# Optimization experiments

Hardware: AMD Instinct MI355X
Metric: run time of the kernel (lower is better)

Reference implementation:

```python
import jax, jax.numpy as jnp
import numpy as np

N_NODES = 100000
N_EDGES = 1000000
IN, HID, HEADS, OUT = 256, 32, 4, 40
HH = HID * HEADS  # 128
NEG_SLOPE = 0.2


def gat_conv(x, W, al, ar, b, src, dst, heads):
    """DGL-style GATConv. x:[N,Din] W:[Din,heads*F] al/ar/b:[heads,F]. Returns [N,heads,F]."""
    N = x.shape[0]
    h = (x @ W).reshape(N, heads, -1)                      # [N,H,F]
    el = (h * al).sum(-1)                                  # [N,H]
    er = (h * ar).sum(-1)                                  # [N,H]
    e = jax.nn.leaky_relu(el[src] + er[dst], NEG_SLOPE)    # [E,H]
    # segment softmax over incoming edges of each dst node
    m = jax.ops.segment_max(e, dst, num_segments=N)        # [N,H]
    m = jnp.where(jnp.isfinite(m), m, 0.0)                 # nodes w/o in-edges
    ex = jnp.exp(e - m[dst])                               # [E,H]
    s = jax.ops.segment_sum(ex, dst, num_segments=N)       # [N,H]
    alpha = ex / jnp.where(s[dst] == 0, 1.0, s[dst])       # [E,H]
    out = jax.ops.segment_sum(alpha[:, :, None] * h[src], dst, num_segments=N)
    return out + b                                          # [N,H,F]


def setup_inputs() -> dict:
    key = jax.random.key(0)
    ks = jax.random.split(key, 12)
    p = lambda k, shape, fan: jax.random.normal(k, shape, jnp.float32) / np.float32(np.sqrt(fan))
    features = jax.random.normal(ks[0], (N_NODES, IN), jnp.float32)
    src = jax.random.randint(ks[1], (N_EDGES,), 0, N_NODES, jnp.int32)
    dst = jax.random.randint(ks[2], (N_EDGES,), 0, N_NODES, jnp.int32)
    W1 = p(ks[3], (IN, HH), IN)
    al1 = p(ks[4], (HEADS, HID), HID)
    ar1 = p(ks[5], (HEADS, HID), HID)
    b1 = jnp.zeros((HEADS, HID), jnp.float32)
    W2 = p(ks[6], (HH, HH), HH)
    al2 = p(ks[7], (HEADS, HID), HID)
    ar2 = p(ks[8], (HEADS, HID), HID)
    b2 = jnp.zeros((HEADS, HID), jnp.float32)
    W3 = p(ks[9], (HH, OUT), HH)
    al3 = p(ks[10], (1, OUT), OUT)
    ar3 = p(ks[11], (1, OUT), OUT)
    b3 = jnp.zeros((1, OUT), jnp.float32)
    return dict(features=features, W1=W1, al1=al1, ar1=ar1, b1=b1,
                W2=W2, al2=al2, ar2=ar2, b2=b2,
                W3=W3, al3=al3, ar3=ar3, b3=b3, src=src, dst=dst)


def reference(features, W1, al1, ar1, b1, W2, al2, ar2, b2, W3, al3, ar3, b3, src, dst):
    N = features.shape[0]
    h = jax.nn.relu(gat_conv(features, W1, al1, ar1, b1, src, dst, HEADS).reshape(N, -1))
    h = jax.nn.relu(gat_conv(h, W2, al2, ar2, b2, src, dst, HEADS).reshape(N, -1))
    # dropout: eval mode -> identity
    h = gat_conv(h, W3, al3, ar3, b3, src, dst, 1).mean(1)  # [N,OUT]
    return jax.nn.log_softmax(h, axis=1)
```

## Files before the change

kernel.cpp:

```cpp
#include <hip/hip_runtime.h>
#include <hip/hip_bf16.h>
#include <math.h>

#define NN 100000
#define NE 1000000
#define NPB 512
#define NBUC ((NN + NPB - 1) / NPB)
#define CAPB 8192
#define P1B 512
#define P1E ((NE + P1B - 1) / P1B)
#define BCAP 512

typedef __attribute__((ext_vector_type(8))) short bf16x8;
typedef __attribute__((ext_vector_type(4))) float f32x4;
typedef unsigned int u32;
typedef unsigned short u16;
typedef unsigned long long u64;

__device__ __forceinline__ u16 f2b(float f) {
    __hip_bfloat16 h = __float2bfloat16(f);
    return *reinterpret_cast<u16*>(&h);
}
__device__ __forceinline__ float b2f(u16 u) {
    __hip_bfloat16 h = *reinterpret_cast<__hip_bfloat16*>(&u);
    return __bfloat162float(h);
}
__device__ __forceinline__ float bflo(u32 v) { return __uint_as_float(v << 16); }
__device__ __forceinline__ float bfhi(u32 v) { return __uint_as_float(v & 0xffff0000u); }


__global__ void bucket_cnt(const int* __restrict__ dst, int* __restrict__ bcnt, int E) {
    __shared__ int c[NBUC];
    for (int i = threadIdx.x; i < NBUC; i += 256) c[i] = 0;
    __syncthreads();
    int i = blockIdx.x * 256 + threadIdx.x;
    const int stride = gridDim.x * 256;
    for (; i < E; i += stride) atomicAdd(&c[dst[i] >> 9], 1);
    __syncthreads();
    for (int j = threadIdx.x; j < NBUC; j += 256)
        if (c[j]) atomicAdd(&bcnt[j], c[j]);
}

__global__ void bucket_scan(const int* __restrict__ bcnt, int* __restrict__ bbase,
                            int* __restrict__ gcur) {
    __shared__ int s[256];
    const int tid = threadIdx.x;
    int v = (tid < NBUC) ? bcnt[tid] : 0;
    s[tid] = v;
    __syncthreads();
    for (int off = 1; off < 256; off <<= 1) {
        int t = (tid >= off) ? s[tid - off] : 0;
        __syncthreads();
        s[tid] += t;
        __syncthreads();
    }
    if (tid < NBUC) {
        int excl = s[tid] - v;
        bbase[tid] = excl;
        gcur[tid] = excl;
    }
    if (tid == NBUC - 1) bbase[NBUC] = s[tid];
}


__global__ __launch_bounds__(256) void part1(const int* __restrict__ src,
                                             const int* __restrict__ dst,
                                             int* __restrict__ gcur,
                                             long long* __restrict__ ebuf) {
    __shared__ int cnt[256], sex[256], base[256], cur2[256], scn[256];
    __shared__ long long stage[P1E];
    const int tid = threadIdx.x;
    const int e0 = blockIdx.x * P1E;
    const int e1 = min(e0 + P1E, NE);
    cnt[tid] = 0;
    __syncthreads();
    for (int i = e0 + tid; i < e1; i += 256)
        atomicAdd(&cnt[dst[i] >> 9], 1);
    __syncthreads();
    int v = cnt[tid];
    scn[tid] = v;
    __syncthreads();
    #pragma unroll
    for (int off = 1; off < 256; off <<= 1) {
        int t = (tid >= off) ? scn[tid - off] : 0;
        __syncthreads();
        scn[tid] += t;
        __syncthreads();
    }
    sex[tid] = scn[tid] - v;
    if (tid < NBUC) base[tid] = (v > 0) ? atomicAdd(&gcur[tid], v) : 0;
    cur2[tid] = 0;
    __syncthreads();
    for (int i = e0 + tid; i < e1; i += 256) {
        int d = dst[i], s = src[i];
        int b = d >> 9;
        int slot = sex[b] + atomicAdd(&cur2[b], 1);
        stage[slot] = ((long long)(u32)d << 32) | (u32)s;
    }
    __syncthreads();
    const int tot = e1 - e0;
    for (int i = tid; i < tot; i += 256) {
        long long ll = stage[i];
        int b = (int)((u64)ll >> 32) >> 9;
        ebuf[(size_t)base[b] + (i - sex[b])] = ll;
    }
}

__global__ __launch_bounds__(256) void part2B(const int* __restrict__ bbase,
                                              const long long* __restrict__ ebuf,
                                              int* __restrict__ rowptr,
                                              int* __restrict__ csrc) {
    __shared__ int nb[NPB], cnt[NPB];
    __shared__ int stage[CAPB];
    __shared__ int ssum[256];
    const int tid = threadIdx.x;
    const int n0 = blockIdx.x << 9;
    const int nn = min(NPB, NN - n0);
    const int estart = bbase[blockIdx.x];
    const int eend = bbase[blockIdx.x + 1];
    const int tot = eend - estart;
    for (int i = tid; i < NPB; i += 256) cnt[i] = 0;
    __syncthreads();
    for (int i = estart + tid; i < eend; i += 256) {
        int ln = (int)((u64)ebuf[i] >> 32) - n0;
        atomicAdd(&cnt[ln], 1);
    }
    __syncthreads();
    int a = cnt[2 * tid], b = cnt[2 * tid + 1];
    int ts = a + b;
    ssum[tid] = ts;
    __syncthreads();
    #pragma unroll
    for (int off = 1; off < 256; off <<= 1) {
        int t = (tid >= off) ? ssum[tid - off] : 0;
        __syncthreads();
        ssum[tid] += t;
        __syncthreads();
    }
    int eb = ssum[tid] - ts;
    nb[2 * tid] = eb;
    nb[2 * tid + 1] = eb + a;
    if (2 * tid < nn)     rowptr[n0 + 2 * tid]     = estart + eb;
    if (2 * tid + 1 < nn) rowptr[n0 + 2 * tid + 1] = estart + eb + a;
    if (tid == 0 && blockIdx.x == gridDim.x - 1) rowptr[NN] = eend;
    __syncthreads();
    for (int i = tid; i < NPB; i += 256) cnt[i] = 0;
    __syncthreads();
    if (tot <= CAPB) {
        for (int i = estart + tid; i < eend; i += 256) {
            long long ll = ebuf[i];
            int ln = (int)((u64)ll >> 32) - n0;
            int pos = nb[ln] + atomicAdd(&cnt[ln], 1);
            stage[pos] = (int)ll;
        }
        __syncthreads();
        for (int i = tid; i < tot; i += 256) csrc[estart + i] = stage[i];
    } else {
        for (int i = estart + tid; i < eend; i += 256) {
            long long ll = ebuf[i];
            int ln = (int)((u64)ll >> 32) - n0;
            int pos = nb[ln] + atomicAdd(&cnt[ln], 1);
            csrc[estart + pos] = (int)ll;
        }
    }
}


__global__ void transW3(const float* __restrict__ W1, u16* __restrict__ W1t,
                        const float* __restrict__ W2, u16* __restrict__ W2t,
                        const float* __restrict__ W3, u16* __restrict__ W3t) {
    int idx = blockIdx.x * 256 + threadIdx.x;
    if (idx < 32768) {
        int n = idx / 256, k = idx % 256;
        W1t[idx] = f2b(W1[(size_t)k * 128 + n]);
    } else if (idx < 32768 + 16384) {
        int j = idx - 32768;
        int n = j / 128, k = j % 128;
        W2t[j] = f2b(W2[(size_t)k * 128 + n]);
    } else if (idx < 32768 + 16384 + 6144) {
        int j = idx - 32768 - 16384;
        int n = j / 128, k = j % 128;
        W3t[j] = f2b((n < 40) ? W3[(size_t)k * 40 + n] : 0.f);
    }
}

template<int K, int NT, int OUTW, bool AF32, int NH>
__global__ __launch_bounds__(256, 4) void gemm_s(const void* __restrict__ Ap_,
                                                 const u16* __restrict__ Wt,
                                                 const float* __restrict__ al,
                                                 const float* __restrict__ ar,
                                                 u16* __restrict__ C,
                                                 float* __restrict__ el,
                                                 float* __restrict__ er, int M) {
    constexpr int KC = 128;
    constexpr int NKC = K / KC;
    constexpr int NB = NT * 16;
    constexpr int CHK = KC / 8;
    __shared__ u16 lB[NB * KC];
    const int tid = threadIdx.x;
    const int w = tid >> 6, l = tid & 63;
    const int lr = l & 15, lq = l >> 4;
    const int row0 = blockIdx.x * 64 + w * 16;
    const u16* Ab = (const u16*)Ap_;
    const float* Af = (const float*)Ap_;

    int gr0 = row0 + lr; if (gr0 >= M) gr0 = M - 1;
    const size_t aoff = (size_t)gr0 * K;

    f32x4 acc[NT] = {};
    #pragma unroll
    for (int kc = 0; kc < NKC; ++kc) {
        for (int idx = tid; idx < NB * CHK; idx += 256) {
            int row = idx / CHK, c = idx % CHK;
            float4 v = *reinterpret_cast<const float4*>(&Wt[(size_t)row * K + kc * KC + c * 8]);
            int cs = c ^ (row & 7);
            *reinterpret_cast<float4*>(&lB[row * KC + cs * 8]) = v;
        }
        __syncthreads();
        bf16x8 a0, a1, a2, a3;
        if (AF32) {
            float4 v[8];
            #pragma unroll
            for (int i = 0; i < 8; ++i)
                v[i] = *reinterpret_cast<const float4*>(
                    &Af[aoff + kc * KC + (i >> 1) * 32 + lq * 8 + (i & 1) * 4]);
            bf16x8 t[4];
            #pragma unroll
            for (int i = 0; i < 4; ++i) {
                t[i][0] = (short)f2b(v[2 * i].x); t[i][1] = (short)f2b(v[2 * i].y);
                t[i][2] = (short)f2b(v[2 * i].z); t[i][3] = (short)f2b(v[2 * i].w);
                t[i][4] = (short)f2b(v[2 * i + 1].x); t[i][5] = (short)f2b(v[2 * i + 1].y);
                t[i][6] = (short)f2b(v[2 * i + 1].z); t[i][7] = (short)f2b(v[2 * i + 1].w);
            }
            a0 = t[0]; a1 = t[1]; a2 = t[2]; a3 = t[3];
        } else {
            a0 = *reinterpret_cast<const bf16x8*>(&Ab[aoff + kc * KC + 0 * 32 + lq * 8]);
            a1 = *reinterpret_cast<const bf16x8*>(&Ab[aoff + kc * KC + 1 * 32 + lq * 8]);
            a2 = *reinterpret_cast<const bf16x8*>(&Ab[aoff + kc * KC + 2 * 32 + lq * 8]);
            a3 = *reinterpret_cast<const bf16x8*>(&Ab[aoff + kc * KC + 3 * 32 + lq * 8]);
        }
        #pragma unroll
        for (int ks = 0; ks < 4; ++ks) {
            bf16x8 aF = (ks == 0) ? a0 : (ks == 1) ? a1 : (ks == 2) ? a2 : a3;
            const int cs = (ks * 4 + lq) ^ (lr & 7);
            #pragma unroll
            for (int nr = 0; nr < NT; ++nr) {
                bf16x8 bF = *reinterpret_cast<const bf16x8*>(&lB[(nr * 16 + lr) * KC + cs * 8]);
                acc[nr] = __builtin_amdgcn_mfma_f32_16x16x32_bf16(aF, bF, acc[nr], 0, 0, 0);
            }
        }
        if (kc + 1 < NKC) __syncthreads();
    }

    float alv[NT], arv[NT];
    #pragma unroll
    for (int nr = 0; nr < NT; ++nr) {
        int c = nr * 16 + lr;
        alv[nr] = (c < OUTW) ? al[c] : 0.f;
        arv[nr] = (c < OUTW) ? ar[c] : 0.f;
    }
    #pragma unroll
    for (int reg = 0; reg < 4; ++reg) {
        int gr = row0 + lq * 4 + reg;
        bool ok = gr < M;
        if (ok) {
            #pragma unroll
            for (int nr = 0; nr < NT; ++nr) {
                int gc = nr * 16 + lr;
                if (gc < OUTW) C[(size_t)gr * OUTW + gc] = f2b(acc[nr][reg]);
            }
        }
        float pl[NH] = {}, pr[NH] = {};
        #pragma unroll
        for (int nr = 0; nr < NT; ++nr) {
            int hidx = (NH == 1) ? 0 : (nr >> 1);
            pl[hidx] = fmaf(acc[nr][reg], alv[nr], pl[hidx]);
            pr[hidx] = fmaf(acc[nr][reg], arv[nr], pr[hidx]);
        }
        #pragma unroll
        for (int o = 8; o >= 1; o >>= 1) {
            #pragma unroll
            for (int hh = 0; hh < NH; ++hh) {
                pl[hh] += __shfl_xor(pl[hh], o);
                pr[hh] += __shfl_xor(pr[hh], o);
            }
        }
        if (ok && lr == 0) {
            #pragma unroll
            for (int hh = 0; hh < NH; ++hh) {
                el[gr * NH + hh] = pl[hh];
                er[gr * NH + hh] = pr[hh];
            }
        }
    }
}


template<bool RELU>
__global__ __launch_bounds__(256) void agg4v6(const char* __restrict__ hbase,
                                              const float4* __restrict__ el4,
                                              const float4* __restrict__ er4,
                                              const float* __restrict__ bias,
                                              const int* __restrict__ rowptr,
                                              const int* __restrict__ csrc,
                                              u32* __restrict__ out, int N) {
    __shared__ u32 s_ed[BCAP][8];
    __shared__ int s_off[9];
    const int tid = threadIdx.x, w = tid >> 6, lane = tid & 63;
    const int base = blockIdx.x * 8;
    if (tid < 9) {
        int n = base + tid;
        s_off[tid] = rowptr[n <= N ? n : N];
    }
    __syncthreads();
    const int beg_blk = s_off[0];
    const int T = s_off[8] - beg_blk;
    const int hh = lane >> 4;
    const u32 lshl = (u32)(lane << 2);
    const float2 bv = reinterpret_cast<const float2*>(bias)[lane];
    const bool small = (T <= BCAP);

    if (small) {
        for (int t = tid; t < T; t += 256) {
            int sid = csrc[beg_blk + t];
            int nd = 0;
            #pragma unroll
            for (int k = 1; k < 8; ++k) nd += (t >= (s_off[k] - beg_blk)) ? 1 : 0;
            float4 er = er4[base + nd];
            float4 ev = el4[sid];
            float e0 = ev.x + er.x; e0 = e0 > 0.f ? e0 : 0.2f * e0;
            float e1 = ev.y + er.y; e1 = e1 > 0.f ? e1 : 0.2f * e1;
            float e2 = ev.z + er.z; e2 = e2 > 0.f ? e2 : 0.2f * e2;
            float e3 = ev.w + er.w; e3 = e3 > 0.f ? e3 : 0.2f * e3;
            u32 so = (u32)sid << 8;
            *reinterpret_cast<int2*>(&s_ed[t][0]) = make_int2(__float_as_int(__expf(e0)), (int)so);
            *reinterpret_cast<int2*>(&s_ed[t][2]) = make_int2(__float_as_int(__expf(e1)), (int)so);
            *reinterpret_cast<int2*>(&s_ed[t][4]) = make_int2(__float_as_int(__expf(e2)), (int)so);
            *reinterpret_cast<int2*>(&s_ed[t][6]) = make_int2(__float_as_int(__expf(e3)), (int)so);
        }
    }
    __syncthreads();

    const int nA = base + 2 * w;
    if (nA >= N) return;
    const int nB = nA + 1;
    float aA[4] = {}, bA[4] = {}, sA[4] = {};
    float aB[4] = {}, bB[4] = {}, sB[4] = {};

    if (small) {
        const int oA0 = s_off[2 * w] - beg_blk, oA1 = s_off[2 * w + 1] - beg_blk;
        const int oB0 = oA1, oB1 = s_off[2 * w + 2] - beg_blk;
        const int dA = oA1 - oA0, dB = oB1 - oB0;
        const int it = max((dA + 3) >> 2, (dB + 3) >> 2);
        for (int i = 0; i < it; ++i) {
            const int pA = oA0 + i * 4, pB = oB0 + i * 4;
            #pragma unroll
            for (int k = 0; k < 4; ++k) {
                int j = pA + k; bool v = j < oA1;
                int2 rv = *reinterpret_cast<const int2*>(&s_ed[v ? j : 0][hh * 2]);
                float wg = v ? __int_as_float(rv.x) : 0.f;
                u32 hv = *reinterpret_cast<const u32*>(hbase + ((u32)rv.y | lshl));
                aA[k] = fmaf(wg, bflo(hv), aA[k]);
                bA[k] = fmaf(wg, bfhi(hv), bA[k]);
                sA[k] += wg;
            }
            #pragma unroll
            for (int k = 0; k < 4; ++k) {
                int j = pB + k; bool v = j < oB1;
                int2 rv = *reinterpret_cast<const int2*>(&s_ed[v ? j : 0][hh * 2]);
                float wg = v ? __int_as_float(rv.x) : 0.f;
                u32 hv = *reinterpret_cast<const u32*>(hbase + ((u32)rv.y | lshl));
                aB[k] = fmaf(wg, bflo(hv), aB[k]);
                bB[k] = fmaf(wg, bfhi(hv), bB[k]);
                sB[k] += wg;
            }
        }
        {
            float accA = (aA[0] + aA[1]) + (aA[2] + aA[3]);
            float accB = (bA[0] + bA[1]) + (bA[2] + bA[3]);
            float s = (sA[0] + sA[1]) + (sA[2] + sA[3]);
            float invs = (dA > 0) ? 1.f / s : 0.f;
            float oA = accA * invs + bv.x;
            float oB = accB * invs + bv.y;
            if (RELU) { oA = fmaxf(oA, 0.f); oB = fmaxf(oB, 0.f); }
            out[(size_t)nA * 64 + lane] = ((u32)f2b(oB) << 16) | (u32)f2b(oA);
        }
        {
            float accA = (aB[0] + aB[1]) + (aB[2] + aB[3]);
            float accB = (bB[0] + bB[1]) + (bB[2] + bB[3]);
            float s = (sB[0] + sB[1]) + (sB[2] + sB[3]);
            float invs = (dB > 0) ? 1.f / s : 0.f;
            float oA = accA * invs + bv.x;
            float oB = accB * invs + bv.y;
            if (RELU) { oA = fmaxf(oA, 0.f); oB = fmaxf(oB, 0.f); }
            if (nB < N)
                out[(size_t)nB * 64 + lane] = ((u32)f2b(oB) << 16) | (u32)f2b(oA);
        }
    } else {
        #pragma unroll
        for (int which = 0; which < 2; ++which) {
            int nd = nA + which;
            if (nd >= N) break;
            int beg = s_off[2 * w + which], end = s_off[2 * w + which + 1];
            float4 er = er4[nd];
            float er_h = hh == 0 ? er.x : hh == 1 ? er.y : hh == 2 ? er.z : er.w;
            float s = 0.f, accA = 0.f, accB = 0.f;
            for (int q = beg; q < end; ++q) {
                int sid = csrc[q];
                float4 ev = el4[sid];
                float e = (hh == 0 ? ev.x : hh == 1 ? ev.y : hh == 2 ? ev.z : ev.w) + er_h;
                e = e > 0.f ? e : 0.2f * e;
                float pe = __expf(e);
                u32 hv = *reinterpret_cast<const u32*>(hbase + (((u32)sid << 8) | lshl));
                s += pe;
                accA = fmaf(pe, bflo(hv), accA);
                accB = fmaf(pe, bfhi(hv), accB);
            }
            float invs = (end > beg) ? 1.f / s : 0.f;
            float oA = accA * invs + bv.x;
            float oB = accB * invs + bv.y;
            if (RELU) { oA = fmaxf(oA, 0.f); oB = fmaxf(oB, 0.f); }
            out[(size_t)nd * 64 + lane] = ((u32)f2b(oB) << 16) | (u32)f2b(oA);
        }
    }
}

__global__ __launch_bounds__(256) void agg1v6(const char* __restrict__ hbase,
                                              const float* __restrict__ el,
                                              const float* __restrict__ er,
                                              const float* __restrict__ bias,
                                              const int* __restrict__ rowptr,
                                              const int* __restrict__ csrc,
                                              float* __restrict__ out, int N) {
    __shared__ u32 s_e1[BCAP][2];
    __shared__ int s_off[9];
    const int tid = threadIdx.x, w = tid >> 6, lane = tid & 63;
    const int base = blockIdx.x * 8;
    if (tid < 9) {
        int n = base + tid;
        s_off[tid] = rowptr[n <= N ? n : N];
    }
    __syncthreads();
    const int beg_blk = s_off[0];
    const int T = s_off[8] - beg_blk;
    const int ll = lane < 40 ? lane : 39;
    const u32 lloff = (u32)(ll << 1);
    const float bvv = (lane < 40) ? bias[lane] : 0.f;
    const bool small = (T <= BCAP);

    if (small) {
        for (int t = tid; t < T; t += 256) {
            int sid = csrc[beg_blk + t];
            int nd = 0;
            #pragma unroll
            for (int k = 1; k < 8; ++k) nd += (t >= (s_off[k] - beg_blk)) ? 1 : 0;
            float e = el[sid] + er[base + nd];
            e = e > 0.f ? e : 0.2f * e;
            *reinterpret_cast<int2*>(&s_e1[t][0]) =
                make_int2(__float_as_int(__expf(e)), (int)((u32)sid * 80u));
        }
    }
    __syncthreads();

    const int nA = base + 2 * w;
    if (nA >= N) return;
    const int nB = nA + 1;
    float aA[4] = {}, sA[4] = {}, aB[4] = {}, sB[4] = {};
    float accA, invsA, accB, invsB;
    bool haveB = (nB < N);

    if (small) {
        const int oA0 = s_off[2 * w] - beg_blk, oA1 = s_off[2 * w + 1] - beg_blk;
        const int oB0 = oA1, oB1 = s_off[2 * w + 2] - beg_blk;
        const int dA = oA1 - oA0, dB = oB1 - oB0;
        const int it = max((dA + 3) >> 2, (dB + 3) >> 2);
        for (int i = 0; i < it; ++i) {
            const int pA = oA0 + i * 4, pB = oB0 + i * 4;
            #pragma unroll
            for (int k = 0; k < 4; ++k) {
                int j = pA + k; bool v = j < oA1;
                int2 rv = *reinterpret_cast<const int2*>(&s_e1[v ? j : 0][0]);
                float wg = v ? __int_as_float(rv.x) : 0.f;
                u16 hv = *reinterpret_cast<const u16*>(hbase + ((u32)rv.y + lloff));
                aA[k] = fmaf(wg, b2f(hv), aA[k]);
                sA[k] += wg;
            }
            #pragma unroll
            for (int k = 0; k < 4; ++k) {
                int j = pB + k; bool v = j < oB1;
                int2 rv = *reinterpret_cast<const int2*>(&s_e1[v ? j : 0][0]);
                float wg = v ? __int_as_float(rv.x) : 0.f;
                u16 hv = *reinterpret_cast<const u16*>(hbase + ((u32)rv.y + lloff));
                aB[k] = fmaf(wg, b2f(hv), aB[k]);
                sB[k] += wg;
            }
        }
        accA = (aA[0] + aA[1]) + (aA[2] + aA[3]);
        float ssA = (sA[0] + sA[1]) + (sA[2] + sA[3]);
        invsA = (dA > 0) ? 1.f / ssA : 0.f;
        accB = (aB[0] + aB[1]) + (aB[2] + aB[3]);
        float ssB = (sB[0] + sB[1]) + (sB[2] + sB[3]);
        invsB = (dB > 0) ? 1.f / ssB : 0.f;
    } else {
        accA = 0.f; accB = 0.f; invsA = 0.f; invsB = 0.f;
        #pragma unroll
        for (int which = 0; which < 2; ++which) {
            int nd = nA + which;
            if (nd >= N) break;
            int beg = s_off[2 * w + which], end = s_off[2 * w + which + 1];
            float ern = er[nd];
            float s = 0.f, acc = 0.f;
            for (int q = beg; q < end; ++q) {
                int sid = csrc[q];
                float e = el[sid] + ern; e = e > 0.f ? e : 0.2f * e;
                float pe = __expf(e);
                u16 hv = *reinterpret_cast<const u16*>(hbase + ((u32)sid * 80u + lloff));
                s += pe;
                acc = fmaf(pe, b2f(hv), acc);
            }
            float inv = (end > beg) ? 1.f / s : 0.f;
            if (which == 0) { accA = acc; invsA = inv; }
            else { accB = acc; invsB = inv; }
        }
    }
    {
        float v = accA * invsA + bvv;
        float vv = (lane < 40) ? v : -INFINITY;
        float mx = vv;
        #pragma unroll
        for (int o = 32; o >= 1; o >>= 1) mx = fmaxf(mx, __shfl_xor(mx, o));
        float ex = (lane < 40) ? __expf(v - mx) : 0.f;
        float se = ex;
        #pragma unroll
        for (int o = 32; o >= 1; o >>= 1) se += __shfl_xor(se, o);
        if (lane < 40) out[(size_t)nA * 40 + lane] = v - mx - logf(se);
    }
    if (haveB) {
        float v = accB * invsB + bvv;
        float vv = (lane < 40) ? v : -INFINITY;
        float mx = vv;
        #pragma unroll
        for (int o = 32; o >= 1; o >>= 1) mx = fmaxf(mx, __shfl_xor(mx, o));
        float ex = (lane < 40) ? __expf(v - mx) : 0.f;
        float se = ex;
        #pragma unroll
        for (int o = 32; o >= 1; o >>= 1) se += __shfl_xor(se, o);
        if (lane < 40) out[(size_t)nB * 40 + lane] = v - mx - logf(se);
    }
}


extern "C" void kernel_launch(void* const* d_in, const int* in_sizes, int n_in,
                              void* d_out, int out_size, void* d_ws, size_t ws_size,
                              hipStream_t stream) {
    const float* feat = (const float*)d_in[0];
    const float* W1  = (const float*)d_in[1];
    const float* al1 = (const float*)d_in[2];
    const float* ar1 = (const float*)d_in[3];
    const float* b1  = (const float*)d_in[4];
    const float* W2  = (const float*)d_in[5];
    const float* al2 = (const float*)d_in[6];
    const float* ar2 = (const float*)d_in[7];
    const float* b2  = (const float*)d_in[8];
    const float* W3  = (const float*)d_in[9];
    const float* al3 = (const float*)d_in[10];
    const float* ar3 = (const float*)d_in[11];
    const float* b3  = (const float*)d_in[12];
    const int*   src = (const int*)d_in[13];
    const int*   dst = (const int*)d_in[14];
    float* out = (float*)d_out;
    const int N = NN, E = NE;

    char* ws = (char*)d_ws;
    size_t off = 0;
    auto alloc = [&](size_t bytes) -> char* {
        char* p = ws + off;
        off += (bytes + 255) & ~(size_t)255;
        return p;
    };
    int* bcnt   = (int*)alloc(256 * 4);
    int* bbase  = (int*)alloc(256 * 4);
    int* gcur   = (int*)alloc(256 * 4);
    int* rowptr = (int*)alloc((size_t)(N + 1) * 4);
    int* csrc   = (int*)alloc((size_t)E * 4);
    long long* ebuf = (long long*)alloc((size_t)E * 8);
    float* el   = (float*)alloc((size_t)N * 4 * 4);
    float* er   = (float*)alloc((size_t)N * 4 * 4);
    u16* hb     = (u16*)alloc((size_t)N * 128 * 2);
    u16* xb     = (u16*)alloc((size_t)N * 128 * 2);
    u16* h3     = (u16*)alloc((size_t)N * 40 * 2 + 256);
    u16* W1t    = (u16*)alloc((size_t)128 * 256 * 2);
    u16* W2t    = (u16*)alloc((size_t)128 * 128 * 2);
    u16* W3t    = (u16*)alloc((size_t)48 * 128 * 2);

    hipMemsetAsync(bcnt, 0, NBUC * 4, stream);
    bucket_cnt<<<1024, 256, 0, stream>>>(dst, bcnt, E);
    bucket_scan<<<1, 256, 0, stream>>>(bcnt, bbase, gcur);
    part1<<<P1B, 256, 0, stream>>>(src, dst, gcur, ebuf);
    part2B<<<NBUC, 256, 0, stream>>>(bbase, ebuf, rowptr, csrc);

    transW3<<<(32768 + 16384 + 6144 + 255) / 256, 256, 0, stream>>>(W1, W1t, W2, W2t, W3, W3t);

    int gemmGrid = (N + 63) / 64;
    int aggGrid = (N + 7) / 8;

    gemm_s<256, 8, 128, true, 4><<<gemmGrid, 256, 0, stream>>>(feat, W1t, al1, ar1, hb, el, er, N);
    agg4v6<true><<<aggGrid, 256, 0, stream>>>((const char*)hb, (const float4*)el, (const float4*)er,
                                              b1, rowptr, csrc, (u32*)xb, N);

    gemm_s<128, 8, 128, false, 4><<<gemmGrid, 256, 0, stream>>>(xb, W2t, al2, ar2, hb, el, er, N);
    agg4v6<true><<<aggGrid, 256, 0, stream>>>((const char*)hb, (const float4*)el, (const float4*)er,
                                              b2, rowptr, csrc, (u32*)xb, N);

    gemm_s<128, 3, 40, false, 1><<<gemmGrid, 256, 0, stream>>>(xb, W3t, al3, ar3, h3, el, er, N);
    agg1v6<<<aggGrid, 256, 0, stream>>>((const char*)h3, el, er, b3, rowptr, csrc, out, N);
}
```

Before: 268.7 us.

## Make GEMM persistent with full weight matrix resident in LDS

```diff
diff --git a/kernel.cpp b/kernel.cpp
--- a/kernel.cpp
+++ b/kernel.cpp
@@ -10,6 +10,7 @@
 #define P1B 512
 #define P1E ((NE + P1B - 1) / P1B)
 #define BCAP 512
+#define GEMM_GB 782
 
 typedef __attribute__((ext_vector_type(8))) short bf16x8;
 typedef __attribute__((ext_vector_type(4))) float f32x4;
@@ -185,7 +186,7 @@
 }
 
 template<int K, int NT, int OUTW, bool AF32, int NH>
-__global__ __launch_bounds__(256, 4) void gemm_s(const void* __restrict__ Ap_,
+__global__ __launch_bounds__(256, 2) void gemm_p(const void* __restrict__ Ap_,
                                                  const u16* __restrict__ Wt,
                                                  const float* __restrict__ al,
                                                  const float* __restrict__ ar,
@@ -195,62 +196,22 @@
     constexpr int KC = 128;
     constexpr int NKC = K / KC;
     constexpr int NB = NT * 16;
-    constexpr int CHK = KC / 8;
-    __shared__ u16 lB[NB * KC];
+    constexpr int CHKF = K / 8;
+    __shared__ u16 lB[NB * K];
     const int tid = threadIdx.x;
     const int w = tid >> 6, l = tid & 63;
     const int lr = l & 15, lq = l >> 4;
-    const int row0 = blockIdx.x * 64 + w * 16;
     const u16* Ab = (const u16*)Ap_;
     const float* Af = (const float*)Ap_;
-
-    int gr0 = row0 + lr; if (gr0 >= M) gr0 = M - 1;
-    const size_t aoff = (size_t)gr0 * K;
-
-    f32x4 acc[NT] = {};
-    #pragma unroll
-    for (int kc = 0; kc < NKC; ++kc) {
-        for (int idx = tid; idx < NB * CHK; idx += 256) {
-            int row = idx / CHK, c = idx % CHK;
-            float4 v = *reinterpret_cast<const float4*>(&Wt[(size_t)row * K + kc * KC + c * 8]);
-            int cs = c ^ (row & 7);
-            *reinterpret_cast<float4*>(&lB[row * KC + cs * 8]) = v;
-        }
-        __syncthreads();
-        bf16x8 a0, a1, a2, a3;
-        if (AF32) {
-            float4 v[8];
-            #pragma unroll
-            for (int i = 0; i < 8; ++i)
-                v[i] = *reinterpret_cast<const float4*>(
-                    &Af[aoff + kc * KC + (i >> 1) * 32 + lq * 8 + (i & 1) * 4]);
-            bf16x8 t[4];
-            #pragma unroll
-            for (int i = 0; i < 4; ++i) {
-                t[i][0] = (short)f2b(v[2 * i].x); t[i][1] = (short)f2b(v[2 * i].y);
-                t[i][2] = (short)f2b(v[2 * i].z); t[i][3] = (short)f2b(v[2 * i].w);
-                t[i][4] = (short)f2b(v[2 * i + 1].x); t[i][5] = (short)f2b(v[2 * i + 1].y);
-                t[i][6] = (short)f2b(v[2 * i + 1].z); t[i][7] = (short)f2b(v[2 * i + 1].w);
-            }
-            a0 = t[0]; a1 = t[1]; a2 = t[2]; a3 = t[3];
-        } else {
-            a0 = *reinterpret_cast<const bf16x8*>(&Ab[aoff + kc * KC + 0 * 32 + lq * 8]);
-            a1 = *reinterpret_cast<const bf16x8*>(&Ab[aoff + kc * KC + 1 * 32 + lq * 8]);
-            a2 = *reinterpret_cast<const bf16x8*>(&Ab[aoff + kc * KC + 2 * 32 + lq * 8]);
-            a3 = *reinterpret_cast<const bf16x8*>(&Ab[aoff + kc * KC + 3 * 32 + lq * 8]);
-        }
-        #pragma unroll
-        for (int ks = 0; ks < 4; ++ks) {
-            bf16x8 aF = (ks == 0) ? a0 : (ks == 1) ? a1 : (ks == 2) ? a2 : a3;
-            const int cs = (ks * 4 + lq) ^ (lr & 7);
-            #pragma unroll
-            for (int nr = 0; nr < NT; ++nr) {
-                bf16x8 bF = *reinterpret_cast<const bf16x8*>(&lB[(nr * 16 + lr) * KC + cs * 8]);
-                acc[nr] = __builtin_amdgcn_mfma_f32_16x16x32_bf16(aF, bF, acc[nr], 0, 0, 0);
-            }
-        }
-        if (kc + 1 < NKC) __syncthreads();
-    }
+    const int numTiles = (M + 63) / 64;
+
+    for (int idx = tid; idx < NB * CHKF; idx += 256) {
+        int row = idx / CHKF, c = idx % CHKF;
+        float4 v = *reinterpret_cast<const float4*>(&Wt[(size_t)row * K + c * 8]);
+        int cs = c ^ (row & 7);
+        *reinterpret_cast<float4*>(&lB[row * K + cs * 8]) = v;
+    }
+    __syncthreads();
 
     float alv[NT], arv[NT];
     #pragma unroll
@@ -259,37 +220,81 @@
         alv[nr] = (c < OUTW) ? al[c] : 0.f;
         arv[nr] = (c < OUTW) ? ar[c] : 0.f;
     }
-    #pragma unroll
-    for (int reg = 0; reg < 4; ++reg) {
-        int gr = row0 + lq * 4 + reg;
-        bool ok = gr < M;
-        if (ok) {
+
+    for (int t = blockIdx.x; t < numTiles; t += GEMM_GB) {
+        const int row0 = t * 64 + w * 16;
+        int gr0 = row0 + lr; if (gr0 >= M) gr0 = M - 1;
+        const size_t aoff = (size_t)gr0 * K;
+
+        f32x4 acc[NT] = {};
+        #pragma unroll
+        for (int kc = 0; kc < NKC; ++kc) {
+            bf16x8 a0, a1, a2, a3;
+            if (AF32) {
+                float4 v[8];
+                #pragma unroll
+                for (int i = 0; i < 8; ++i)
+                    v[i] = *reinterpret_cast<const float4*>(
+                        &Af[aoff + kc * KC + (i >> 1) * 32 + lq * 8 + (i & 1) * 4]);
+                bf16x8 tt[4];
+                #pragma unroll
+                for (int i = 0; i < 4; ++i) {
+                    tt[i][0] = (short)f2b(v[2 * i].x); tt[i][1] = (short)f2b(v[2 * i].y);
+                    tt[i][2] = (short)f2b(v[2 * i].z); tt[i][3] = (short)f2b(v[2 * i].w);
+                    tt[i][4] = (short)f2b(v[2 * i + 1].x); tt[i][5] = (short)f2b(v[2 * i + 1].y);
+                    tt[i][6] = (short)f2b(v[2 * i + 1].z); tt[i][7] = (short)f2b(v[2 * i + 1].w);
+                }
+                a0 = tt[0]; a1 = tt[1]; a2 = tt[2]; a3 = tt[3];
+            } else {
+                a0 = *reinterpret_cast<const bf16x8*>(&Ab[aoff + kc * KC + 0 * 32 + lq * 8]);
+                a1 = *reinterpret_cast<const bf16x8*>(&Ab[aoff + kc * KC + 1 * 32 + lq * 8]);
+                a2 = *reinterpret_cast<const bf16x8*>(&Ab[aoff + kc * KC + 2 * 32 + lq * 8]);
+                a3 = *reinterpret_cast<const bf16x8*>(&Ab[aoff + kc * KC + 3 * 32 + lq * 8]);
+            }
+            #pragma unroll
+            for (int ks = 0; ks < 4; ++ks) {
+                bf16x8 aF = (ks == 0) ? a0 : (ks == 1) ? a1 : (ks == 2) ? a2 : a3;
+                const int cs = ((kc * 16 + ks * 4 + lq) ^ (lr & 7));
+                #pragma unroll
+                for (int nr = 0; nr < NT; ++nr) {
+                    bf16x8 bF = *reinterpret_cast<const bf16x8*>(&lB[(nr * 16 + lr) * K + cs * 8]);
+                    acc[nr] = __builtin_amdgcn_mfma_f32_16x16x32_bf16(aF, bF, acc[nr], 0, 0, 0);
+                }
+            }
+        }
+
+        #pragma unroll
+        for (int reg = 0; reg < 4; ++reg) {
+            int gr = row0 + lq * 4 + reg;
+            bool ok = gr < M;
+            if (ok) {
+                #pragma unroll
+                for (int nr = 0; nr < NT; ++nr) {
+                    int gc = nr * 16 + lr;
+                    if (gc < OUTW) C[(size_t)gr * OUTW + gc] = f2b(acc[nr][reg]);
+                }
+            }
+            float pl[NH] = {}, pr[NH] = {};
             #pragma unroll
             for (int nr = 0; nr < NT; ++nr) {
-                int gc = nr * 16 + lr;
-                if (gc < OUTW) C[(size_t)gr * OUTW + gc] = f2b(acc[nr][reg]);
-            }
-        }
-        float pl[NH] = {}, pr[NH] = {};
-        #pragma unroll
-        for (int nr = 0; nr < NT; ++nr) {
-            int hidx = (NH == 1) ? 0 : (nr >> 1);
-            pl[hidx] = fmaf(acc[nr][reg], alv[nr], pl[hidx]);
-            pr[hidx] = fmaf(acc[nr][reg], arv[nr], pr[hidx]);
-        }
-        #pragma unroll
-        for (int o = 8; o >= 1; o >>= 1) {
-            #pragma unroll
-            for (int hh = 0; hh < NH; ++hh) {
-                pl[hh] += __shfl_xor(pl[hh], o);
-                pr[hh] += __shfl_xor(pr[hh], o);
-            }
-        }
-        if (ok && lr == 0) {
-            #pragma unroll
-            for (int hh = 0; hh < NH; ++hh) {
-                el[gr * NH + hh] = pl[hh];
-                er[gr * NH + hh] = pr[hh];
+                int hidx = (NH == 1) ? 0 : (nr >> 1);
+                pl[hidx] = fmaf(acc[nr][reg], alv[nr], pl[hidx]);
+                pr[hidx] = fmaf(acc[nr][reg], arv[nr], pr[hidx]);
+            }
+            #pragma unroll
+            for (int o = 8; o >= 1; o >>= 1) {
+                #pragma unroll
+                for (int hh = 0; hh < NH; ++hh) {
+                    pl[hh] += __shfl_xor(pl[hh], o);
+                    pr[hh] += __shfl_xor(pr[hh], o);
+                }
+            }
+            if (ok && lr == 0) {
+                #pragma unroll
+                for (int hh = 0; hh < NH; ++hh) {
+                    el[gr * NH + hh] = pl[hh];
+                    er[gr * NH + hh] = pr[hh];
+                }
             }
         }
     }
@@ -601,17 +606,16 @@
 
     transW3<<<(32768 + 16384 + 6144 + 255) / 256, 256, 0, stream>>>(W1, W1t, W2, W2t, W3, W3t);
 
-    int gemmGrid = (N + 63) / 64;
     int aggGrid = (N + 7) / 8;
 
-    gemm_s<256, 8, 128, true, 4><<<gemmGrid, 256, 0, stream>>>(feat, W1t, al1, ar1, hb, el, er, N);
+    gemm_p<256, 8, 128, true, 4><<<GEMM_GB, 256, 0, stream>>>(feat, W1t, al1, ar1, hb, el, er, N);
     agg4v6<true><<<aggGrid, 256, 0, stream>>>((const char*)hb, (const float4*)el, (const float4*)er,
                                               b1, rowptr, csrc, (u32*)xb, N);
 
-    gemm_s<128, 8, 128, false, 4><<<gemmGrid, 256, 0, stream>>>(xb, W2t, al2, ar2, hb, el, er, N);
+    gemm_p<128, 8, 128, false, 4><<<GEMM_GB, 256, 0, stream>>>(xb, W2t, al2, ar2, hb, el, er, N);
     agg4v6<true><<<aggGrid, 256, 0, stream>>>((const char*)hb, (const float4*)el, (const float4*)er,
                                               b2, rowptr, csrc, (u32*)xb, N);
 
-    gemm_s<128, 3, 40, false, 1><<<gemmGrid, 256, 0, stream>>>(xb, W3t, al3, ar3, h3, el, er, N);
+    gemm_p<128, 3, 40, false, 1><<<GEMM_GB, 256, 0, stream>>>(xb, W3t, al3, ar3, h3, el, er, N);
     agg1v6<<<aggGrid, 256, 0, stream>>>((const char*)h3, el, er, b3, rowptr, csrc, out, N);
 }
```

Result: slower. 317.8 us (+18.3%).
